# Optimization experiments

Hardware: AMD Instinct MI355X
Metric: run time of the kernel (lower is better)

Reference implementation:

```python
import jax, jax.numpy as jnp
import numpy as np

K = 8  # FLAGS.num_neighbors


def _knn_project(verts, pc_coords, pc_feat):
    """One projected_neighborhood stage.
    verts:     [N, 3]   mesh vertices (queries)
    pc_coords: [1, 3, M] point-cloud coordinates
    pc_feat:   [1, Df, M] point-cloud features
    Returns (coord_out [N,3], feat_out [N,Df]).
    """
    pts = pc_coords[0].T            # [M, 3]
    feats = pc_feat[0].T            # [M, Df]
    x2 = jnp.sum(verts * verts, axis=1, keepdims=True)      # [N, 1]
    y2 = jnp.sum(pts * pts, axis=1)[None, :]                 # [1, M]
    d2 = jnp.maximum(x2 + y2 - 2.0 * (verts @ pts.T), 0.0)   # [N, M]
    _, idx = jax.lax.top_k(-d2, K)                            # [N, K] nearest
    nbr = pts[idx]                                            # [N, K, 3]
    vec = nbr - verts[:, None, :]                             # vec_to_neighbors
    dist2 = jnp.sum(vec * vec, axis=2)                        # knn_dist^2 [N, K]
    w = 1.0 / (1.0 + dist2)                                   # inverse_square_dist weight
    coord_out = jnp.mean(vec * w[:, :, None], axis=1) + verts
    feat_out = jnp.mean(feats[idx] * w[:, :, None], axis=1)   # [N, Df]
    return coord_out, feat_out


def setup_inputs() -> dict:
    key = jax.random.key(0)
    ks = jax.random.split(key, 8)
    return {
        "inputs": jax.random.normal(ks[0], (4096, 3), dtype=jnp.float32),
        "pc0_coords": jax.random.normal(ks[1], (1, 3, 32768), dtype=jnp.float32),
        "pc1_coords": jax.random.normal(ks[2], (1, 3, 32768), dtype=jnp.float32),
        "pc1_feat": jax.random.normal(ks[3], (1, 64, 32768), dtype=jnp.float32),
        "pc2_coords": jax.random.normal(ks[4], (1, 3, 16384), dtype=jnp.float32),
        "pc2_feat": jax.random.normal(ks[5], (1, 128, 16384), dtype=jnp.float32),
        "pc3_coords": jax.random.normal(ks[6], (1, 3, 8192), dtype=jnp.float32),
        "pc3_feat": jax.random.normal(ks[7], (1, 256, 8192), dtype=jnp.float32),
    }


def reference(inputs, pc0_coords, pc1_coords, pc1_feat, pc2_coords, pc2_feat,
              pc3_coords, pc3_feat):
    # NOTE: the original computes stage_0 (coords only, features==coords) but
    # discards it; the output only uses stages 1..3 features. We skip it.
    _, f1 = _knn_project(inputs, pc1_coords, pc1_feat)
    _, f2 = _knn_project(inputs, pc2_coords, pc2_feat)
    _, f3 = _knn_project(inputs, pc3_coords, pc3_feat)
    return jnp.concatenate([inputs, f1, f2, f3], axis=1)  # [N, 3+64+128+256]
```

## Files before the change

### kernel.cpp

```cpp
#include <hip/hip_runtime.h>
#include <float.h>

#define NV 4096
#define OSTRIDE 451
#define NT 256
#define PK1OFF 6291456
#define PK2OFF (6291456 + 131072)
#define PK3OFF (6291456 + 196608)
#define MARGIN 1e-3f
typedef unsigned long long u64;

struct Top8 {
    unsigned d0,d1,d2,d3,d4,d5,d6,d7;
    int      i0,i1,i2,i3,i4,i5,i6,i7;
};

__device__ __forceinline__ void top8_init(Top8& t) {
    t.d0=t.d1=t.d2=t.d3=t.d4=t.d5=t.d6=t.d7=0x7F7FFFFFu;
    t.i0=t.i1=t.i2=t.i3=t.i4=t.i5=t.i6=t.i7=0x7fffffff;
}

__device__ __forceinline__ void ins8s(Top8& t, unsigned cd, int cm) {
    bool b0 = cd < t.d0, b1 = cd < t.d1, b2 = cd < t.d2, b3 = cd < t.d3;
    bool b4 = cd < t.d4, b5 = cd < t.d5, b6 = cd < t.d6;
    t.d7 = b6 ? t.d6 : cd;                 t.i7 = b6 ? t.i6 : cm;
    t.d6 = b5 ? t.d5 : (b6 ? cd : t.d6);   t.i6 = b5 ? t.i5 : (b6 ? cm : t.i6);
    t.d5 = b4 ? t.d4 : (b5 ? cd : t.d5);   t.i5 = b4 ? t.i4 : (b5 ? cm : t.i5);
    t.d4 = b3 ? t.d3 : (b4 ? cd : t.d4);   t.i4 = b3 ? t.i3 : (b4 ? cm : t.i4);
    t.d3 = b2 ? t.d2 : (b3 ? cd : t.d3);   t.i3 = b2 ? t.i2 : (b3 ? cm : t.i3);
    t.d2 = b1 ? t.d1 : (b2 ? cd : t.d2);   t.i2 = b1 ? t.i1 : (b2 ? cm : t.i2);
    t.d1 = b0 ? t.d0 : (b1 ? cd : t.d1);   t.i1 = b0 ? t.i0 : (b1 ? cm : t.i1);
    t.d0 = b0 ? cd : t.d0;                 t.i0 = b0 ? cm : t.i0;
}

__device__ __forceinline__ void handle_s(u64 mask, float dj, int ibase,
                                         Top8& t, float& Tf) {
    while (mask) {
        int l = __builtin_ctzll(mask);
        mask &= mask - 1;
        int cm = ibase + l;
        if (cm < 8) continue;
        unsigned cd = (unsigned)__builtin_amdgcn_readlane(__float_as_uint(dj), l);
        if (cd < t.d7) {
            ins8s(t, cd, cm);
            Tf = __uint_as_float(t.d7);
            mask &= __ballot(dj < Tf);
        }
    }
}

template<int M>
__device__ __forceinline__ float wcalc(const float* __restrict__ pc, int m,
                                       float vx, float vy, float vz) {
    float qx = pc[m], qy = pc[M+m], qz = pc[2*M+m];
    float dx = __fsub_rn(qx, vx), dy = __fsub_rn(qy, vy), dz = __fsub_rn(qz, vz);
    float dist2 = __fadd_rn(__fadd_rn(__fmul_rn(dx,dx), __fmul_rn(dy,dy)),
                            __fmul_rn(dz,dz));
    return __fdiv_rn(1.0f, __fadd_rn(1.0f, dist2));
}

template<int M, int DF, int COFF, bool TR, bool PK>
__device__ __forceinline__ void stage2v(
    const float* __restrict__ verts,
    const float* __restrict__ pc,
    const float* __restrict__ feat,
    const float* __restrict__ featT,
    const float4* __restrict__ pk,
    float* __restrict__ out,
    int vbase, int lane)
{
    float vx[2], vy[2], vz[2];
#pragma unroll
    for (int u = 0; u < 2; ++u) {
        vx[u] = verts[(vbase+u)*3+0];
        vy[u] = verts[(vbase+u)*3+1];
        vz[u] = verts[(vbase+u)*3+2];
    }

    Top8 t0, t1;
    top8_init(t0); top8_init(t1);
#pragma unroll
    for (int q = 0; q < 8; ++q) {
        float sx = pc[q], sy = pc[M+q], sz = pc[2*M+q];
        {
            float dx=__fsub_rn(sx,vx[0]), dy=__fsub_rn(sy,vy[0]), dz=__fsub_rn(sz,vz[0]);
            float d = __fmaf_rn(dz,dz,__fmaf_rn(dy,dy,__fmul_rn(dx,dx)));
            unsigned cd = (unsigned)__builtin_amdgcn_readfirstlane(__float_as_uint(d));
            if (cd < t0.d7) ins8s(t0, cd, q);
        }
        {
            float dx=__fsub_rn(sx,vx[1]), dy=__fsub_rn(sy,vy[1]), dz=__fsub_rn(sz,vz[1]);
            float d = __fmaf_rn(dz,dz,__fmaf_rn(dy,dy,__fmul_rn(dx,dx)));
            unsigned cd = (unsigned)__builtin_amdgcn_readfirstlane(__float_as_uint(d));
            if (cd < t1.d7) ins8s(t1, cd, q);
        }
    }
    float T[2];
    T[0] = __uint_as_float(t0.d7);
    T[1] = __uint_as_float(t1.d7);

    float c0[2], c1[2], c2[2], v2m[2], Tg[2];
    if constexpr (PK) {
#pragma unroll
        for (int u = 0; u < 2; ++u) {
            c0[u] = __fmul_rn(-2.0f, vx[u]);
            c1[u] = __fmul_rn(-2.0f, vy[u]);
            c2[u] = __fmul_rn(-2.0f, vz[u]);
            float v2 = __fadd_rn(__fadd_rn(__fmul_rn(vx[u],vx[u]), __fmul_rn(vy[u],vy[u])),
                                 __fmul_rn(vz[u],vz[u]));
            v2m[u] = __fsub_rn(v2, MARGIN);
            Tg[u]  = __fsub_rn(T[u], v2m[u]);
        }
    }

    const float* __restrict__ px = pc;
    const float* __restrict__ py = pc + M;
    const float* __restrict__ pz = pc + 2*M;

    if constexpr (PK) {
        float4 cp[4];
#pragma unroll
        for (int j = 0; j < 4; ++j) cp[j] = pk[64*j + lane];

        for (int ob = 0; ob < M; ob += 256) {
            int nb = (ob + 256 < M) ? ob + 256 : 0;
            float4 np[4];
#pragma unroll
            for (int j = 0; j < 4; ++j) np[j] = pk[nb + 64*j + lane];
            float s0[4], s1[4];
#pragma unroll
            for (int j = 0; j < 4; ++j) {
                s0[j] = __fmaf_rn(cp[j].x, c0[0], __fmaf_rn(cp[j].y, c1[0],
                        __fmaf_rn(cp[j].z, c2[0], cp[j].w)));
                s1[j] = __fmaf_rn(cp[j].x, c0[1], __fmaf_rn(cp[j].y, c1[1],
                        __fmaf_rn(cp[j].z, c2[1], cp[j].w)));
            }
            u64 g0[4], g1[4]; u64 any = 0;
#pragma unroll
            for (int j = 0; j < 4; ++j) {
                g0[j] = __ballot(s0[j] < Tg[0]);
                g1[j] = __ballot(s1[j] < Tg[1]);
                any |= g0[j] | g1[j];
            }
            if (any) {
#pragma unroll
                for (int j = 0; j < 4; ++j) {
                    if (g0[j]) {
                        float dx = __fsub_rn(cp[j].x, vx[0]);
                        float dy = __fsub_rn(cp[j].y, vy[0]);
                        float dz = __fsub_rn(cp[j].z, vz[0]);
                        float d2x = __fmaf_rn(dz,dz,__fmaf_rn(dy,dy,__fmul_rn(dx,dx)));
                        u64 em = __ballot(d2x < T[0]);
                        if (em) {
                            handle_s(em, d2x, ob + 64*j, t0, T[0]);
                            Tg[0] = __fsub_rn(T[0], v2m[0]);
                        }
                    }
                }
#pragma unroll
                for (int j = 0; j < 4; ++j) {
                    if (g1[j]) {
                        float dx = __fsub_rn(cp[j].x, vx[1]);
                        float dy = __fsub_rn(cp[j].y, vy[1]);
                        float dz = __fsub_rn(cp[j].z, vz[1]);
                        float d2x = __fmaf_rn(dz,dz,__fmaf_rn(dy,dy,__fmul_rn(dx,dx)));
                        u64 em = __ballot(d2x < T[1]);
                        if (em) {
                            handle_s(em, d2x, ob + 64*j, t1, T[1]);
                            Tg[1] = __fsub_rn(T[1], v2m[1]);
                        }
                    }
                }
            }
#pragma unroll
            for (int j = 0; j < 4; ++j) cp[j] = np[j];
        }
    } else {
        float cx[4], cy[4], cz[4];
#pragma unroll
        for (int j = 0; j < 4; ++j) {
            cx[j] = px[64*j + lane]; cy[j] = py[64*j + lane]; cz[j] = pz[64*j + lane];
        }
        for (int ob = 0; ob < M; ob += 256) {
            int nb = (ob + 256 < M) ? ob + 256 : 0;
            float nx[4], ny[4], nz[4];
#pragma unroll
            for (int j = 0; j < 4; ++j) {
                nx[j] = px[nb + 64*j + lane];
                ny[j] = py[nb + 64*j + lane];
                nz[j] = pz[nb + 64*j + lane];
            }
            float d[2][4];
#pragma unroll
            for (int u = 0; u < 2; ++u)
#pragma unroll
                for (int j = 0; j < 4; ++j) {
                    float dx = __fsub_rn(cx[j], vx[u]);
                    float dy = __fsub_rn(cy[j], vy[u]);
                    float dz = __fsub_rn(cz[j], vz[u]);
                    d[u][j] = __fmaf_rn(dz,dz,__fmaf_rn(dy,dy,__fmul_rn(dx,dx)));
                }
            u64 msk[2][4]; u64 any = 0;
#pragma unroll
            for (int u = 0; u < 2; ++u)
#pragma unroll
                for (int j = 0; j < 4; ++j) {
                    msk[u][j] = __ballot(d[u][j] < T[u]);
                    any |= msk[u][j];
                }
            if (any) {
#pragma unroll
                for (int j = 0; j < 4; ++j)
                    handle_s(msk[0][j], d[0][j], ob + 64*j, t0, T[0]);
#pragma unroll
                for (int j = 0; j < 4; ++j)
                    handle_s(msk[1][j], d[1][j], ob + 64*j, t1, T[1]);
            }
#pragma unroll
            for (int j = 0; j < 4; ++j) { cx[j]=nx[j]; cy[j]=ny[j]; cz[j]=nz[j]; }
        }
    }

    int m8[2][8];
    m8[0][0]=t0.i0; m8[0][1]=t0.i1; m8[0][2]=t0.i2; m8[0][3]=t0.i3;
    m8[0][4]=t0.i4; m8[0][5]=t0.i5; m8[0][6]=t0.i6; m8[0][7]=t0.i7;
    m8[1][0]=t1.i0; m8[1][1]=t1.i1; m8[1][2]=t1.i2; m8[1][3]=t1.i3;
    m8[1][4]=t1.i4; m8[1][5]=t1.i5; m8[1][6]=t1.i6; m8[1][7]=t1.i7;
#pragma unroll
    for (int u = 0; u < 2; ++u) {
        float w8[8];
#pragma unroll
        for (int k = 0; k < 8; ++k)
            w8[k] = wcalc<M>(pc, m8[u][k], vx[u], vy[u], vz[u]);
        const int n = vbase + u;
        for (int f = lane; f < DF; f += 64) {
            float e[8];
#pragma unroll
            for (int k = 0; k < 8; ++k) {
                float fv = TR ? featT[m8[u][k]*DF + f] : feat[f*M + m8[u][k]];
                e[k] = __fmul_rn(w8[k], fv);
            }
            float s = __fadd_rn(__fadd_rn(__fadd_rn(e[0],e[1]), __fadd_rn(e[2],e[3])),
                                __fadd_rn(__fadd_rn(e[4],e[5]), __fadd_rn(e[6],e[7])));
            out[n*OSTRIDE + COFF + f] = __fmul_rn(0.125f, s);
        }
    }
}

__global__ __launch_bounds__(256)
void tr_kernel(const float* __restrict__ f1, const float* __restrict__ f2,
               const float* __restrict__ f3,
               const float* __restrict__ pc1, const float* __restrict__ pc2,
               const float* __restrict__ pc3, float* __restrict__ ws)
{
    int b = blockIdx.x;
    if (b >= 1536) {
        int g = (b - 1536)*256 + threadIdx.x;
        float x, y, z; float4* dst;
        if (g < 32768)      { x=pc1[g];      y=pc1[32768+g];  z=pc1[65536+g];  dst=(float4*)(ws+PK1OFF)+g; }
        else if (g < 49152) { int m=g-32768; x=pc2[m]; y=pc2[16384+m]; z=pc2[32768+m]; dst=(float4*)(ws+PK2OFF)+m; }
        else                { int m=g-49152; x=pc3[m]; y=pc3[8192+m];  z=pc3[16384+m]; dst=(float4*)(ws+PK3OFF)+m; }
        float pn = __fmaf_rn(z,z,__fmaf_rn(y,y,__fmul_rn(x,x)));
        *dst = make_float4(x, y, z, pn);
        return;
    }
    __shared__ float s[64][65];
    const float* src; float* dst; int M, DF, tm, tf;
    if (b < 512)       { src = f1; dst = ws;           M = 32768; DF = 64;  tm = b & 511;        tf = b >> 9; }
    else if (b < 1024) { src = f2; dst = ws + 2097152; M = 16384; DF = 128; tm = (b-512) & 255;  tf = (b-512) >> 8; }
    else               { src = f3; dst = ws + 4194304; M = 8192;  DF = 256; tm = (b-1024) & 127; tf = (b-1024) >> 7; }
    const int mb = tm*64, fb = tf*64;
    const int tid = threadIdx.x;
    const int a0 = tid & 63, a1 = tid >> 6;
#pragma unroll
    for (int i = 0; i < 16; ++i) {
        int ff = a1 + i*4;
        s[ff][a0] = src[(fb+ff)*M + mb + a0];
    }
    __syncthreads();
#pragma unroll
    for (int i = 0; i < 16; ++i) {
        int mm2 = a1 + i*4;
        dst[(mb+mm2)*DF + fb + a0] = s[a0][mm2];
    }
}

template<bool TR, bool PK>
__global__ __launch_bounds__(NT, 6)
void gp_kernel(const float* __restrict__ verts,
               const float* __restrict__ pc1, const float* __restrict__ f1,
               const float* __restrict__ pc2, const float* __restrict__ f2,
               const float* __restrict__ pc3, const float* __restrict__ f3,
               const float* __restrict__ ws,
               float* __restrict__ out)
{
    int b = blockIdx.x;
    if (b < 1536) {
        const int lane = threadIdx.x & 63;
        const int wv   = threadIdx.x >> 6;
        if (b < 512) {
            stage2v<32768,  64,   3, TR, PK>(verts, pc1, f1, ws,
                (const float4*)(ws+PK1OFF), out, (b*4 + wv)*2, lane);
        } else if (b < 1024) {
            stage2v<16384, 128,  67, TR, PK>(verts, pc2, f2, ws + 2097152,
                (const float4*)(ws+PK2OFF), out, ((b-512)*4 + wv)*2, lane);
        } else {
            stage2v< 8192, 256, 195, TR, PK>(verts, pc3, f3, ws + 4194304,
                (const float4*)(ws+PK3OFF), out, ((b-1024)*4 + wv)*2, lane);
        }
    } else {
        for (int i = threadIdx.x; i < NV*3; i += NT)
            out[(i/3)*OSTRIDE + (i % 3)] = verts[i];
    }
}

extern "C" void kernel_launch(void* const* d_in, const int* in_sizes, int n_in,
                              void* d_out, int out_size, void* d_ws, size_t ws_size,
                              hipStream_t stream) {
    const float* verts = (const float*)d_in[0];
    const float* pc1 = (const float*)d_in[2];
    const float* f1  = (const float*)d_in[3];
    const float* pc2 = (const float*)d_in[4];
    const float* f2  = (const float*)d_in[5];
    const float* pc3 = (const float*)d_in[6];
    const float* f3  = (const float*)d_in[7];
    float* out = (float*)d_out;
    float* ws  = (float*)d_ws;

    const size_t need_tr = 6291456ull * 4ull;
    const size_t need_pk = (6291456ull + 229376ull) * 4ull;
    if (ws_size >= need_pk) {
        tr_kernel<<<1760, 256, 0, stream>>>(f1, f2, f3, pc1, pc2, pc3, ws);
        gp_kernel<true, true><<<1537, NT, 0, stream>>>(verts, pc1, f1, pc2, f2, pc3, f3, ws, out);
    } else if (ws_size >= need_tr) {
        tr_kernel<<<1536, 256, 0, stream>>>(f1, f2, f3, pc1, pc2, pc3, ws);
        gp_kernel<true, false><<<1537, NT, 0, stream>>>(verts, pc1, f1, pc2, f2, pc3, f3, ws, out);
    } else {
        gp_kernel<false, false><<<1537, NT, 0, stream>>>(verts, pc1, f1, pc2, f2, pc3, f3, ws, out);
    }
}
```

Baseline: 114.9 us.

## Stage packed point tiles through double-buffered LDS shared by block's waves

The packed-point scan now loads 512-point tiles cooperatively into a double-buffered shared-memory array, and all four waves of the block read them from LDS instead of each wave streaming the points from global memory. The next tile is prefetched into registers while the current one is processed, then stored to the other buffer before a block-wide barrier. This cuts redundant global/L2 traffic by a factor of the wave count. In exchange it adds a __syncthreads per tile, which couples the waves so that a wave slowed by insertions stalls the others, plus 16KB of LDS per block that may limit occupancy.

```diff
diff --git a/kernel.cpp b/kernel.cpp
--- a/kernel.cpp
+++ b/kernel.cpp
@@ -4,6 +4,7 @@
 #define NV 4096
 #define OSTRIDE 451
 #define NT 256
+#define TILE 512
 #define PK1OFF 6291456
 #define PK2OFF (6291456 + 131072)
 #define PK3OFF (6291456 + 196608)
@@ -59,15 +60,16 @@
     return __fdiv_rn(1.0f, __fadd_rn(1.0f, dist2));
 }
 
-template<int M, int DF, int COFF, bool TR, bool PK>
-__device__ __forceinline__ void stage2v(
+template<int M, int DF, int COFF, bool TR>
+__device__ __forceinline__ void stage2v_lds(
     const float* __restrict__ verts,
     const float* __restrict__ pc,
     const float* __restrict__ feat,
     const float* __restrict__ featT,
     const float4* __restrict__ pk,
+    float4 (*sbuf)[TILE],
     float* __restrict__ out,
-    int vbase, int lane)
+    int vbase, int lane, int tid)
 {
     float vx[2], vy[2], vz[2];
 #pragma unroll
@@ -100,33 +102,37 @@
     T[1] = __uint_as_float(t1.d7);
 
     float c0[2], c1[2], c2[2], v2m[2], Tg[2];
-    if constexpr (PK) {
-#pragma unroll
-        for (int u = 0; u < 2; ++u) {
-            c0[u] = __fmul_rn(-2.0f, vx[u]);
-            c1[u] = __fmul_rn(-2.0f, vy[u]);
-            c2[u] = __fmul_rn(-2.0f, vz[u]);
-            float v2 = __fadd_rn(__fadd_rn(__fmul_rn(vx[u],vx[u]), __fmul_rn(vy[u],vy[u])),
-                                 __fmul_rn(vz[u],vz[u]));
-            v2m[u] = __fsub_rn(v2, MARGIN);
-            Tg[u]  = __fsub_rn(T[u], v2m[u]);
-        }
-    }
-
-    const float* __restrict__ px = pc;
-    const float* __restrict__ py = pc + M;
-    const float* __restrict__ pz = pc + 2*M;
-
-    if constexpr (PK) {
-        float4 cp[4];
-#pragma unroll
-        for (int j = 0; j < 4; ++j) cp[j] = pk[64*j + lane];
-
-        for (int ob = 0; ob < M; ob += 256) {
-            int nb = (ob + 256 < M) ? ob + 256 : 0;
-            float4 np[4];
-#pragma unroll
-            for (int j = 0; j < 4; ++j) np[j] = pk[nb + 64*j + lane];
+#pragma unroll
+    for (int u = 0; u < 2; ++u) {
+        c0[u] = __fmul_rn(-2.0f, vx[u]);
+        c1[u] = __fmul_rn(-2.0f, vy[u]);
+        c2[u] = __fmul_rn(-2.0f, vz[u]);
+        float v2 = __fadd_rn(__fadd_rn(__fmul_rn(vx[u],vx[u]), __fmul_rn(vy[u],vy[u])),
+                             __fmul_rn(vz[u],vz[u]));
+        v2m[u] = __fsub_rn(v2, MARGIN);
+        Tg[u]  = __fsub_rn(T[u], v2m[u]);
+    }
+
+    constexpr int NTILE = M / TILE;
+    sbuf[0][tid]       = pk[tid];
+    sbuf[0][tid + 256] = pk[tid + 256];
+    __syncthreads();
+
+    for (int t = 0; t < NTILE; ++t) {
+        const int cur = t & 1;
+        float4 r0, r1;
+        const bool more = (t + 1 < NTILE);
+        if (more) {
+            r0 = pk[(t+1)*TILE + tid];
+            r1 = pk[(t+1)*TILE + tid + 256];
+        }
+#pragma unroll
+        for (int half = 0; half < 2; ++half) {
+            const int ib = t*TILE + half*256;
+            float4 cp[4];
+#pragma unroll
+            for (int j = 0; j < 4; ++j)
+                cp[j] = sbuf[cur][half*256 + 64*j + lane];
             float s0[4], s1[4];
 #pragma unroll
             for (int j = 0; j < 4; ++j) {
@@ -152,7 +158,7 @@
                         float d2x = __fmaf_rn(dz,dz,__fmaf_rn(dy,dy,__fmul_rn(dx,dx)));
                         u64 em = __ballot(d2x < T[0]);
                         if (em) {
-                            handle_s(em, d2x, ob + 64*j, t0, T[0]);
+                            handle_s(em, d2x, ib + 64*j, t0, T[0]);
                             Tg[0] = __fsub_rn(T[0], v2m[0]);
                         }
                     }
@@ -166,59 +172,127 @@
                         float d2x = __fmaf_rn(dz,dz,__fmaf_rn(dy,dy,__fmul_rn(dx,dx)));
                         u64 em = __ballot(d2x < T[1]);
                         if (em) {
-                            handle_s(em, d2x, ob + 64*j, t1, T[1]);
+                            handle_s(em, d2x, ib + 64*j, t1, T[1]);
                             Tg[1] = __fsub_rn(T[1], v2m[1]);
                         }
                     }
                 }
             }
-#pragma unroll
-            for (int j = 0; j < 4; ++j) cp[j] = np[j];
-        }
-    } else {
-        float cx[4], cy[4], cz[4];
+        }
+        if (more) {
+            sbuf[cur ^ 1][tid]       = r0;
+            sbuf[cur ^ 1][tid + 256] = r1;
+        }
+        __syncthreads();
+    }
+
+    int m8[2][8];
+    m8[0][0]=t0.i0; m8[0][1]=t0.i1; m8[0][2]=t0.i2; m8[0][3]=t0.i3;
+    m8[0][4]=t0.i4; m8[0][5]=t0.i5; m8[0][6]=t0.i6; m8[0][7]=t0.i7;
+    m8[1][0]=t1.i0; m8[1][1]=t1.i1; m8[1][2]=t1.i2; m8[1][3]=t1.i3;
+    m8[1][4]=t1.i4; m8[1][5]=t1.i5; m8[1][6]=t1.i6; m8[1][7]=t1.i7;
+#pragma unroll
+    for (int u = 0; u < 2; ++u) {
+        float w8[8];
+#pragma unroll
+        for (int k = 0; k < 8; ++k)
+            w8[k] = wcalc<M>(pc, m8[u][k], vx[u], vy[u], vz[u]);
+        const int n = vbase + u;
+        for (int f = lane; f < DF; f += 64) {
+            float e[8];
+#pragma unroll
+            for (int k = 0; k < 8; ++k) {
+                float fv = TR ? featT[m8[u][k]*DF + f] : feat[f*M + m8[u][k]];
+                e[k] = __fmul_rn(w8[k], fv);
+            }
+            float s = __fadd_rn(__fadd_rn(__fadd_rn(e[0],e[1]), __fadd_rn(e[2],e[3])),
+                                __fadd_rn(__fadd_rn(e[4],e[5]), __fadd_rn(e[6],e[7])));
+            out[n*OSTRIDE + COFF + f] = __fmul_rn(0.125f, s);
+        }
+    }
+}
+
+template<int M, int DF, int COFF, bool TR>
+__device__ __forceinline__ void stage2v(
+    const float* __restrict__ verts,
+    const float* __restrict__ pc, const float* __restrict__ feat,
+    const float* __restrict__ featT, float* __restrict__ out,
+    int vbase, int lane)
+{
+    float vx[2], vy[2], vz[2];
+#pragma unroll
+    for (int u = 0; u < 2; ++u) {
+        vx[u] = verts[(vbase+u)*3+0];
+        vy[u] = verts[(vbase+u)*3+1];
+        vz[u] = verts[(vbase+u)*3+2];
+    }
+    Top8 t0, t1;
+    top8_init(t0); top8_init(t1);
+#pragma unroll
+    for (int q = 0; q < 8; ++q) {
+        float sx = pc[q], sy = pc[M+q], sz = pc[2*M+q];
+        {
+            float dx=__fsub_rn(sx,vx[0]), dy=__fsub_rn(sy,vy[0]), dz=__fsub_rn(sz,vz[0]);
+            float d = __fmaf_rn(dz,dz,__fmaf_rn(dy,dy,__fmul_rn(dx,dx)));
+            unsigned cd = (unsigned)__builtin_amdgcn_readfirstlane(__float_as_uint(d));
+            if (cd < t0.d7) ins8s(t0, cd, q);
+        }
+        {
+            float dx=__fsub_rn(sx,vx[1]), dy=__fsub_rn(sy,vy[1]), dz=__fsub_rn(sz,vz[1]);
+            float d = __fmaf_rn(dz,dz,__fmaf_rn(dy,dy,__fmul_rn(dx,dx)));
+            unsigned cd = (unsigned)__builtin_amdgcn_readfirstlane(__float_as_uint(d));
+            if (cd < t1.d7) ins8s(t1, cd, q);
+        }
+    }
+    float T[2];
+    T[0] = __uint_as_float(t0.d7);
+    T[1] = __uint_as_float(t1.d7);
+
+    const float* __restrict__ px = pc;
+    const float* __restrict__ py = pc + M;
+    const float* __restrict__ pz = pc + 2*M;
+    float cx[4], cy[4], cz[4];
+#pragma unroll
+    for (int j = 0; j < 4; ++j) {
+        cx[j] = px[64*j + lane]; cy[j] = py[64*j + lane]; cz[j] = pz[64*j + lane];
+    }
+    for (int ob = 0; ob < M; ob += 256) {
+        int nb = (ob + 256 < M) ? ob + 256 : 0;
+        float nx[4], ny[4], nz[4];
 #pragma unroll
         for (int j = 0; j < 4; ++j) {
-            cx[j] = px[64*j + lane]; cy[j] = py[64*j + lane]; cz[j] = pz[64*j + lane];
-        }
-        for (int ob = 0; ob < M; ob += 256) {
-            int nb = (ob + 256 < M) ? ob + 256 : 0;
-            float nx[4], ny[4], nz[4];
+            nx[j] = px[nb + 64*j + lane];
+            ny[j] = py[nb + 64*j + lane];
+            nz[j] = pz[nb + 64*j + lane];
+        }
+        float d[2][4];
+#pragma unroll
+        for (int u = 0; u < 2; ++u)
 #pragma unroll
             for (int j = 0; j < 4; ++j) {
-                nx[j] = px[nb + 64*j + lane];
-                ny[j] = py[nb + 64*j + lane];
-                nz[j] = pz[nb + 64*j + lane];
-            }
-            float d[2][4];
-#pragma unroll
-            for (int u = 0; u < 2; ++u)
-#pragma unroll
-                for (int j = 0; j < 4; ++j) {
-                    float dx = __fsub_rn(cx[j], vx[u]);
-                    float dy = __fsub_rn(cy[j], vy[u]);
-                    float dz = __fsub_rn(cz[j], vz[u]);
-                    d[u][j] = __fmaf_rn(dz,dz,__fmaf_rn(dy,dy,__fmul_rn(dx,dx)));
-                }
-            u64 msk[2][4]; u64 any = 0;
-#pragma unroll
-            for (int u = 0; u < 2; ++u)
-#pragma unroll
-                for (int j = 0; j < 4; ++j) {
-                    msk[u][j] = __ballot(d[u][j] < T[u]);
-                    any |= msk[u][j];
-                }
-            if (any) {
-#pragma unroll
-                for (int j = 0; j < 4; ++j)
-                    handle_s(msk[0][j], d[0][j], ob + 64*j, t0, T[0]);
-#pragma unroll
-                for (int j = 0; j < 4; ++j)
-                    handle_s(msk[1][j], d[1][j], ob + 64*j, t1, T[1]);
-            }
-#pragma unroll
-            for (int j = 0; j < 4; ++j) { cx[j]=nx[j]; cy[j]=ny[j]; cz[j]=nz[j]; }
-        }
+                float dx = __fsub_rn(cx[j], vx[u]);
+                float dy = __fsub_rn(cy[j], vy[u]);
+                float dz = __fsub_rn(cz[j], vz[u]);
+                d[u][j] = __fmaf_rn(dz,dz,__fmaf_rn(dy,dy,__fmul_rn(dx,dx)));
+            }
+        u64 msk[2][4]; u64 any = 0;
+#pragma unroll
+        for (int u = 0; u < 2; ++u)
+#pragma unroll
+            for (int j = 0; j < 4; ++j) {
+                msk[u][j] = __ballot(d[u][j] < T[u]);
+                any |= msk[u][j];
+            }
+        if (any) {
+#pragma unroll
+            for (int j = 0; j < 4; ++j)
+                handle_s(msk[0][j], d[0][j], ob + 64*j, t0, T[0]);
+#pragma unroll
+            for (int j = 0; j < 4; ++j)
+                handle_s(msk[1][j], d[1][j], ob + 64*j, t1, T[1]);
+        }
+#pragma unroll
+        for (int j = 0; j < 4; ++j) { cx[j]=nx[j]; cy[j]=ny[j]; cz[j]=nz[j]; }
     }
 
     int m8[2][8];
@@ -294,19 +368,31 @@
                const float* __restrict__ ws,
                float* __restrict__ out)
 {
+    __shared__ float4 sbuf[2][TILE];
     int b = blockIdx.x;
     if (b < 1536) {
-        const int lane = threadIdx.x & 63;
-        const int wv   = threadIdx.x >> 6;
-        if (b < 512) {
-            stage2v<32768,  64,   3, TR, PK>(verts, pc1, f1, ws,
-                (const float4*)(ws+PK1OFF), out, (b*4 + wv)*2, lane);
-        } else if (b < 1024) {
-            stage2v<16384, 128,  67, TR, PK>(verts, pc2, f2, ws + 2097152,
-                (const float4*)(ws+PK2OFF), out, ((b-512)*4 + wv)*2, lane);
+        const int tid  = threadIdx.x;
+        const int lane = tid & 63;
+        const int wv   = tid >> 6;
+        if constexpr (PK) {
+            if (b < 512) {
+                stage2v_lds<32768,  64,   3, TR>(verts, pc1, f1, ws,
+                    (const float4*)(ws+PK1OFF), sbuf, out, (b*4 + wv)*2, lane, tid);
+            } else if (b < 1024) {
+                stage2v_lds<16384, 128,  67, TR>(verts, pc2, f2, ws + 2097152,
+                    (const float4*)(ws+PK2OFF), sbuf, out, ((b-512)*4 + wv)*2, lane, tid);
+            } else {
+                stage2v_lds< 8192, 256, 195, TR>(verts, pc3, f3, ws + 4194304,
+                    (const float4*)(ws+PK3OFF), sbuf, out, ((b-1024)*4 + wv)*2, lane, tid);
+            }
         } else {
-            stage2v< 8192, 256, 195, TR, PK>(verts, pc3, f3, ws + 4194304,
-                (const float4*)(ws+PK3OFF), out, ((b-1024)*4 + wv)*2, lane);
+            if (b < 512) {
+                stage2v<32768,  64,   3, TR>(verts, pc1, f1, ws,           out, (b*4 + wv)*2, lane);
+            } else if (b < 1024) {
+                stage2v<16384, 128,  67, TR>(verts, pc2, f2, ws + 2097152, out, ((b-512)*4 + wv)*2, lane);
+            } else {
+                stage2v< 8192, 256, 195, TR>(verts, pc3, f3, ws + 4194304, out, ((b-1024)*4 + wv)*2, lane);
+            }
         }
     } else {
         for (int i = threadIdx.x; i < NV*3; i += NT)
```

After: 119.5 us. +4.0%, slower.
